# Optimization experiments

Measured on AMD Instinct MI355X. Metric: run time of the kernel, lower is better.

Reference implementation:

```python
import jax, jax.numpy as jnp
import numpy as np

H, D, DK, DV = 8, 512, 64, 64
B, L = 2, 2048
LN_EPS = 1e-5


def setup_inputs() -> dict:
    key = jax.random.key(0)
    ks = jax.random.split(key, 12)
    q = jax.random.normal(ks[0], (B, L, D), jnp.float32)
    k = jax.random.normal(ks[1], (B, L, D), jnp.float32)
    v = jax.random.normal(ks[2], (B, L, D), jnp.float32)
    mask = jax.random.randint(ks[3], (H * B, L, L), 0, 2) > 0
    sq = np.sqrt(2.0 / (D + DK)).astype(np.float32)
    sv = np.sqrt(2.0 / (D + DV)).astype(np.float32)
    Wq = jax.random.normal(ks[4], (H * DK, D), jnp.float32) * sq
    Wk = jax.random.normal(ks[5], (H * DK, D), jnp.float32) * sq
    Wv = jax.random.normal(ks[6], (H * DV, D), jnp.float32) * sv
    xav = np.sqrt(2.0 / (H * DV + D)).astype(np.float32)
    Wfc = jax.random.normal(ks[7], (D, H * DV), jnp.float32) * xav
    bfc = jnp.zeros((D,), jnp.float32)
    gamma = jnp.ones((D,), jnp.float32)
    beta = jnp.zeros((D,), jnp.float32)
    return {"q": q, "k": k, "v": v, "mask": mask, "Wq": Wq, "Wk": Wk,
            "Wv": Wv, "Wfc": Wfc, "bfc": bfc, "gamma": gamma, "beta": beta}


def reference(q, k, v, mask, Wq, Wk, Wv, Wfc, bfc, gamma, beta):
    # dropout in eval mode (identity)
    temperature = jnp.sqrt(jnp.asarray(DK, q.dtype))
    residual = q
    # projections -> (H, B, L, dk/dv), matching permute(2,0,1,3)
    qh = (q @ Wq.T).reshape(B, L, H, DK).transpose(2, 0, 1, 3)
    kh = (k @ Wk.T).reshape(B, L, H, DK).transpose(2, 0, 1, 3)
    vh = (v @ Wv.T).reshape(B, L, H, DV).transpose(2, 0, 1, 3)
    attn = jnp.einsum('hbqd,hbkd->hbqk', qh, kh) / temperature
    m = mask.reshape(H, B, L, L)
    attn = jnp.where(m, jnp.asarray(-1e10, attn.dtype), attn)
    attn = jax.nn.softmax(attn, axis=-1)
    out = jnp.einsum('hbqk,hbkd->hbqd', attn, vh)  # (H,B,L,DV)
    out = out.transpose(1, 2, 0, 3).reshape(B, L, H * DV)
    out = out @ Wfc.T + bfc
    x = out + residual
    mu = jnp.mean(x, axis=-1, keepdims=True)
    var = jnp.var(x, axis=-1, keepdims=True)
    return gamma * (x - mu) * jax.lax.rsqrt(var + LN_EPS) + beta
```

## Files before the change

kernel.cpp:

```cpp
#include <hip/hip_runtime.h>
#include <hip/hip_bf16.h>
#include <cmath>
#include <cstdint>

#define H_ 8
#define B_ 2
#define L_ 2048
#define D_ 512
#define SPLIT_ 4
#define LP 80

typedef __attribute__((ext_vector_type(8))) short short8_t;
typedef __attribute__((ext_vector_type(4))) float float4_t;
typedef __attribute__((ext_vector_type(4))) unsigned short ushort4_t;
typedef __attribute__((ext_vector_type(4))) unsigned int uint4_t;

__device__ __forceinline__ unsigned short bf16u(float f) {
  union { __hip_bfloat16 b; unsigned short u; } c;
  c.b = __float2bfloat16(f);
  return c.u;
}
__device__ __forceinline__ unsigned bf16x2(float lo, float hi) {
  return (unsigned)bf16u(lo) | ((unsigned)bf16u(hi) << 16);
}
__device__ __forceinline__ float bf2f(unsigned short u) {
  union { unsigned u; float f; } c; c.u = (unsigned)u << 16; return c.f;
}

__device__ __forceinline__ unsigned pack8(unsigned long long x) {
  x |= x >> 4; x |= x >> 2; x |= x >> 1;
  x &= 0x0101010101010101ULL;
  return (unsigned)((x * 0x0102040810204080ULL) >> 56);
}

__global__ __launch_bounds__(512)
void proj_gemm(const float* __restrict__ q, const float* __restrict__ k,
               const float* __restrict__ v,
               const float* __restrict__ wq, const float* __restrict__ wk,
               const float* __restrict__ wv,
               unsigned short* __restrict__ Qp, unsigned short* __restrict__ Kp,
               unsigned short* __restrict__ Vt) {
  __shared__ unsigned short As[128][LP];
  __shared__ unsigned short Bs[64][LP];
  const int tid = threadIdx.x, lane = tid & 63, wave = tid >> 6;
  const int g = lane >> 4, qi = lane & 15;
  const int m0 = blockIdx.x * 128, n0 = blockIdx.y * 64;
  const int z = blockIdx.z;
  const float* A = (z == 0) ? q : (z == 1) ? k : v;
  const float* W = (z == 0) ? wq : (z == 1) ? wk : wv;

  float4_t acc[4] = {};
  const int ar = tid >> 2, ac = (tid & 3) * 16;
  const int br = tid >> 3, bc = (tid & 7) * 8;

  for (int kt = 0; kt < 512; kt += 64) {
    const float* src = A + (size_t)(m0 + ar) * 512 + kt + ac;
    float4_t f0 = *(const float4_t*)(src);
    float4_t f1 = *(const float4_t*)(src + 4);
    float4_t f2 = *(const float4_t*)(src + 8);
    float4_t f3 = *(const float4_t*)(src + 12);
    short8_t s0, s1;
    s0[0] = bf16u(f0[0]); s0[1] = bf16u(f0[1]); s0[2] = bf16u(f0[2]); s0[3] = bf16u(f0[3]);
    s0[4] = bf16u(f1[0]); s0[5] = bf16u(f1[1]); s0[6] = bf16u(f1[2]); s0[7] = bf16u(f1[3]);
    s1[0] = bf16u(f2[0]); s1[1] = bf16u(f2[1]); s1[2] = bf16u(f2[2]); s1[3] = bf16u(f2[3]);
    s1[4] = bf16u(f3[0]); s1[5] = bf16u(f3[1]); s1[6] = bf16u(f3[2]); s1[7] = bf16u(f3[3]);
    *(short8_t*)(&As[ar][ac]) = s0;
    *(short8_t*)(&As[ar][ac + 8]) = s1;
    const float* wsrc = W + (size_t)(n0 + br) * 512 + kt + bc;
    float4_t w0 = *(const float4_t*)(wsrc);
    float4_t w1 = *(const float4_t*)(wsrc + 4);
    short8_t sw;
    sw[0] = bf16u(w0[0]); sw[1] = bf16u(w0[1]); sw[2] = bf16u(w0[2]); sw[3] = bf16u(w0[3]);
    sw[4] = bf16u(w1[0]); sw[5] = bf16u(w1[1]); sw[6] = bf16u(w1[2]); sw[7] = bf16u(w1[3]);
    *(short8_t*)(&Bs[br][bc]) = sw;
    __syncthreads();
#pragma unroll
    for (int kk = 0; kk < 2; kk++) {
      const int krow = kk * 32 + g * 8;
      short8_t a = *(const short8_t*)(&As[wave * 16 + qi][krow]);
#pragma unroll
      for (int n = 0; n < 4; n++) {
        short8_t b = *(const short8_t*)(&Bs[n * 16 + qi][krow]);
        acc[n] = __builtin_amdgcn_mfma_f32_16x16x32_bf16(a, b, acc[n], 0, 0, 0);
      }
    }
    __syncthreads();
  }

  const int gmb = m0 + wave * 16 + g * 4;
#pragma unroll
  for (int n = 0; n < 4; n++) {
    int gn = n0 + n * 16 + qi;
    int h = gn >> 6, d = gn & 63;
    if (z == 2) {
      int bb = gmb >> 11, l = gmb & 2047;
      ushort4_t o;
#pragma unroll
      for (int r = 0; r < 4; r++) o[r] = bf16u(acc[n][r]);
      *(ushort4_t*)(Vt + ((size_t)(h * B_ + bb) * 64 + d) * L_ + l) = o;
    } else {
      float sc = (z == 0) ? 0.125f : 1.0f;
      unsigned short* O = (z == 0) ? Qp : Kp;
#pragma unroll
      for (int r = 0; r < 4; r++) {
        int gm = gmb + r;
        int bb = gm >> 11, l = gm & 2047;
        O[((size_t)(h * B_ + bb) * L_ + l) * 64 + d] = bf16u(acc[n][r] * sc);
      }
    }
  }
}

template<int MS>
__device__ __forceinline__ void attn_body(
    const unsigned short* __restrict__ Qp, const unsigned short* __restrict__ Kp,
    const unsigned short* __restrict__ Vt, const unsigned char* __restrict__ mask,
    unsigned short* __restrict__ Opart, float* __restrict__ MLpart,
    unsigned short (*Ks)[64][LP], unsigned short (*Vs)[64][LP]) {
  const int tid = threadIdx.x, lane = tid & 63, wave = tid >> 6;
  const int g = lane >> 4, qi = lane & 15;
  const int hb = blockIdx.y;
  const int sp = blockIdx.z;
  const int k_begin = sp * (L_ / SPLIT_), k_end = k_begin + L_ / SPLIT_;
  const int qg0 = blockIdx.x * 128 + wave * 16;
  const int qg = qg0 + qi;
  const size_t base = (size_t)hb * (L_ * 64);

  const size_t mrowoff = ((size_t)hb * L_ + qg0 + (lane >> 2)) * L_;
  const unsigned char* mb1 = mask + mrowoff + (lane & 3) * 16;
  const unsigned* mb4 = (const unsigned*)mask + mrowoff + (lane & 3) * 16;

  short8_t qf[2];
#pragma unroll
  for (int kk = 0; kk < 2; kk++)
    qf[kk] = *(const short8_t*)(Qp + base + (size_t)qg * 64 + kk * 32 + g * 8);

  float4_t o[4] = {};
  float mrun = -INFINITY, lrun = 0.f;
  const int sr = tid >> 3, sc = (tid & 7) * 8;
  const int srcA = qi * 4;
  const int srcP = qi + 32 * (g & 1);

#define LOADFB(dst, kpos)                                                        \
  do {                                                                           \
    if (MS == 1) {                                                               \
      uint4_t x = *(const uint4_t*)(mb1 + (kpos));                               \
      unsigned long long lo = ((unsigned long long)x[1] << 32) | x[0];           \
      unsigned long long hi = ((unsigned long long)x[3] << 32) | x[2];           \
      dst = pack8(lo) | (pack8(hi) << 8);                                        \
    } else {                                                                     \
      dst = 0;                                                                   \
      _Pragma("unroll")                                                          \
      for (int j = 0; j < 4; j++) {                                              \
        uint4_t x = *(const uint4_t*)(mb4 + (kpos) + j * 4);                     \
        dst |= (((unsigned)(x[0] != 0)) | ((unsigned)(x[1] != 0) << 1) |         \
                ((unsigned)(x[2] != 0) << 2) | ((unsigned)(x[3] != 0) << 3))     \
               << (j * 4);                                                       \
      }                                                                          \
    }                                                                            \
  } while (0)

  short8_t kr, vr;
  unsigned fb1, fb2;
  kr = *(const short8_t*)(Kp + base + (size_t)(k_begin + sr) * 64 + sc);
  vr = *(const short8_t*)(Vt + base + (size_t)sr * L_ + k_begin + sc);
  LOADFB(fb1, k_begin);
  fb2 = 0;
  if (k_begin + 64 < k_end) LOADFB(fb2, k_begin + 64);
  *(short8_t*)(&Ks[0][sr][sc]) = kr;
  *(short8_t*)(&Vs[0][sr][sc]) = vr;
  __syncthreads();

  int bufi = 0;
  for (int k0 = k_begin; k0 < k_end; k0 += 64) {
    const bool has_next = (k0 + 64 < k_end);
    if (has_next) {
      const int kn = k0 + 64;
      kr = *(const short8_t*)(Kp + base + (size_t)(kn + sr) * 64 + sc);
      vr = *(const short8_t*)(Vt + base + (size_t)sr * L_ + kn + sc);
    }
    unsigned fb_cur = fb1;
    fb1 = fb2;
    if (k0 + 128 < k_end) LOADFB(fb2, k0 + 128);

    unsigned nib[4];
#pragma unroll
    for (int t = 0; t < 4; t++)
      nib[t] = ((unsigned)__shfl((int)fb_cur, srcA + t, 64) >> (g * 4)) & 0xFu;

    float4_t st[4] = {};
#pragma unroll
    for (int kk = 0; kk < 2; kk++) {
      const int krow = kk * 32 + g * 8;
#pragma unroll
      for (int t = 0; t < 4; t++) {
        short8_t a = *(const short8_t*)(&Ks[bufi][t * 16 + qi][krow]);
        st[t] = __builtin_amdgcn_mfma_f32_16x16x32_bf16(a, qf[kk], st[t], 0, 0, 0);
      }
    }

    float tmax = -INFINITY;
#pragma unroll
    for (int t = 0; t < 4; t++)
#pragma unroll
      for (int r = 0; r < 4; r++) {
        if ((nib[t] >> r) & 1u) st[t][r] = -1e10f;
        tmax = fmaxf(tmax, st[t][r]);
      }
    tmax = fmaxf(tmax, __shfl_xor(tmax, 16, 64));
    tmax = fmaxf(tmax, __shfl_xor(tmax, 32, 64));

    float nm = fmaxf(mrun, tmax);
    float fac = __expf(mrun - nm);
    mrun = nm;

    float psum = 0.f;
    unsigned w8[4][2];
#pragma unroll
    for (int t = 0; t < 4; t++) {
      float p0 = __expf(st[t][0] - nm);
      float p1 = __expf(st[t][1] - nm);
      float p2 = __expf(st[t][2] - nm);
      float p3 = __expf(st[t][3] - nm);
      psum += (p0 + p1) + (p2 + p3);
      w8[t][0] = bf16x2(p0, p1);
      w8[t][1] = bf16x2(p2, p3);
    }
    psum += __shfl_xor(psum, 16, 64);
    psum += __shfl_xor(psum, 32, 64);
    lrun = lrun * fac + psum;
#pragma unroll
    for (int n2 = 0; n2 < 4; n2++)
#pragma unroll
      for (int r = 0; r < 4; r++) o[n2][r] *= fac;

#pragma unroll
    for (int s = 0; s < 2; s++) {
      unsigned a00 = (unsigned)__shfl((int)w8[2 * s][0],     srcP, 64);
      unsigned a10 = (unsigned)__shfl((int)w8[2 * s + 1][0], srcP, 64);
      unsigned a01 = (unsigned)__shfl((int)w8[2 * s][1],     srcP, 64);
      unsigned a11 = (unsigned)__shfl((int)w8[2 * s + 1][1], srcP, 64);
      unsigned b00 = (unsigned)__shfl((int)w8[2 * s][0],     srcP + 16, 64);
      unsigned b10 = (unsigned)__shfl((int)w8[2 * s + 1][0], srcP + 16, 64);
      unsigned b01 = (unsigned)__shfl((int)w8[2 * s][1],     srcP + 16, 64);
      unsigned b11 = (unsigned)__shfl((int)w8[2 * s + 1][1], srcP + 16, 64);
      const bool hi = (g & 2) != 0;
      union { unsigned u[4]; short8_t s8; } pb;
      pb.u[0] = hi ? a10 : a00;
      pb.u[1] = hi ? a11 : a01;
      pb.u[2] = hi ? b10 : b00;
      pb.u[3] = hi ? b11 : b01;
#pragma unroll
      for (int n2 = 0; n2 < 4; n2++) {
        short8_t a = *(const short8_t*)(&Vs[bufi][n2 * 16 + qi][s * 32 + g * 8]);
        o[n2] = __builtin_amdgcn_mfma_f32_16x16x32_bf16(a, pb.s8, o[n2], 0, 0, 0);
      }
    }

    if (has_next) {
      *(short8_t*)(&Ks[bufi ^ 1][sr][sc]) = kr;
      *(short8_t*)(&Vs[bufi ^ 1][sr][sc]) = vr;
      __syncthreads();
      bufi ^= 1;
    }
  }
#undef LOADFB

  const size_t pb = (((size_t)sp * 16 + hb) * L_ + qg) * 64;
#pragma unroll
  for (int n2 = 0; n2 < 4; n2++) {
    ushort4_t ov;
#pragma unroll
    for (int r = 0; r < 4; r++) ov[r] = bf16u(o[n2][r]);
    *(ushort4_t*)(Opart + pb + n2 * 16 + g * 4) = ov;
  }
  if (lane < 16) {
    float* ml = MLpart + (((size_t)sp * 16 + hb) * L_ + qg) * 2;
    ml[0] = mrun; ml[1] = lrun;
  }
}

__global__ __launch_bounds__(512)
void attn_split(const unsigned short* __restrict__ Qp, const unsigned short* __restrict__ Kp,
                const unsigned short* __restrict__ Vt, const unsigned char* __restrict__ mask,
                unsigned short* __restrict__ Opart, float* __restrict__ MLpart) {
  __shared__ unsigned short Ks[2][64][LP];
  __shared__ unsigned short Vs[2][64][LP];
  unsigned probe = ((const unsigned*)mask)[threadIdx.x & 63];
  if (__any(probe > 1u))
    attn_body<1>(Qp, Kp, Vt, mask, Opart, MLpart, Ks, Vs);
  else
    attn_body<4>(Qp, Kp, Vt, mask, Opart, MLpart, Ks, Vs);
}

__global__ __launch_bounds__(256)
void attn_combine(const unsigned short* __restrict__ Opart, const float* __restrict__ MLpart,
                  unsigned short* __restrict__ Y) {
  int gid = blockIdx.x * 256 + threadIdx.x;
  int dvc = (gid & 7) * 8;
  int hbq = gid >> 3;
  int hb = hbq >> 11, qq = hbq & 2047;
  int h = hb >> 1, bb = hb & 1;
  float m[SPLIT_], l[SPLIT_];
  float M = -INFINITY;
#pragma unroll
  for (int s = 0; s < SPLIT_; s++) {
    const float* ml = MLpart + (((size_t)s * 16 + hb) * L_ + qq) * 2;
    m[s] = ml[0]; l[s] = ml[1];
    M = fmaxf(M, m[s]);
  }
  float denom = 0.f, e[SPLIT_];
#pragma unroll
  for (int s = 0; s < SPLIT_; s++) { e[s] = __expf(m[s] - M); denom += l[s] * e[s]; }
  float inv = 1.0f / denom;
  float acc[8] = {};
#pragma unroll
  for (int s = 0; s < SPLIT_; s++) {
    const unsigned short* p = Opart + (((size_t)s * 16 + hb) * L_ + qq) * 64 + dvc;
    ushort4_t a0 = *(const ushort4_t*)(p);
    ushort4_t a1 = *(const ushort4_t*)(p + 4);
    float w = e[s] * inv;
#pragma unroll
    for (int j = 0; j < 4; j++) {
      acc[j] += bf2f(a0[j]) * w;
      acc[j + 4] += bf2f(a1[j]) * w;
    }
  }
  short8_t ov;
#pragma unroll
  for (int j = 0; j < 8; j++) ov[j] = bf16u(acc[j]);
  *(short8_t*)(Y + ((size_t)(bb * L_ + qq)) * 512 + h * 64 + dvc) = ov;
}

__global__ __launch_bounds__(512)
void fc_gemm(const unsigned short* __restrict__ Yb, const float* __restrict__ wfc,
             const float* __restrict__ resid, const float* __restrict__ bfc,
             float* __restrict__ out) {
  __shared__ unsigned short As[128][LP];
  __shared__ unsigned short Bs[64][LP];
  const int tid = threadIdx.x, lane = tid & 63, wave = tid >> 6;
  const int g = lane >> 4, qi = lane & 15;
  const int m0 = blockIdx.x * 128, n0 = blockIdx.y * 64;
  float4_t acc[4] = {};
  const int ar = tid >> 2, ac = (tid & 3) * 16;
  const int br = tid >> 3, bc = (tid & 7) * 8;

  for (int kt = 0; kt < 512; kt += 64) {
    const unsigned short* src = Yb + (size_t)(m0 + ar) * 512 + kt + ac;
    *(short8_t*)(&As[ar][ac]) = *(const short8_t*)(src);
    *(short8_t*)(&As[ar][ac + 8]) = *(const short8_t*)(src + 8);
    const float* wsrc = wfc + (size_t)(n0 + br) * 512 + kt + bc;
    float4_t w0 = *(const float4_t*)(wsrc);
    float4_t w1 = *(const float4_t*)(wsrc + 4);
    short8_t sw;
    sw[0] = bf16u(w0[0]); sw[1] = bf16u(w0[1]); sw[2] = bf16u(w0[2]); sw[3] = bf16u(w0[3]);
    sw[4] = bf16u(w1[0]); sw[5] = bf16u(w1[1]); sw[6] = bf16u(w1[2]); sw[7] = bf16u(w1[3]);
    *(short8_t*)(&Bs[br][bc]) = sw;
    __syncthreads();
#pragma unroll
    for (int kk = 0; kk < 2; kk++) {
      const int krow = kk * 32 + g * 8;
      short8_t a = *(const short8_t*)(&As[wave * 16 + qi][krow]);
#pragma unroll
      for (int n = 0; n < 4; n++) {
        short8_t b = *(const short8_t*)(&Bs[n * 16 + qi][krow]);
        acc[n] = __builtin_amdgcn_mfma_f32_16x16x32_bf16(a, b, acc[n], 0, 0, 0);
      }
    }
    __syncthreads();
  }

  const int gmb = m0 + wave * 16 + g * 4;
#pragma unroll
  for (int n = 0; n < 4; n++) {
    int gn = n0 + n * 16 + qi;
    float bv = bfc[gn];
#pragma unroll
    for (int r = 0; r < 4; r++) {
      int gm = gmb + r;
      out[(size_t)gm * 512 + gn] = acc[n][r] + bv + resid[(size_t)gm * 512 + gn];
    }
  }
}

__global__ __launch_bounds__(256)
void ln_kernel(float* __restrict__ Z, const float* __restrict__ gamma,
               const float* __restrict__ beta) {
  const int row = blockIdx.x * 4 + (threadIdx.x >> 6);
  const int lane = threadIdx.x & 63;
  float* zp = Z + (size_t)row * 512 + lane * 8;
  float4_t x0 = *(const float4_t*)(zp);
  float4_t x1 = *(const float4_t*)(zp + 4);
  float s = 0.f, s2 = 0.f;
#pragma unroll
  for (int j = 0; j < 4; j++) { s += x0[j] + x1[j]; s2 += x0[j] * x0[j] + x1[j] * x1[j]; }
#pragma unroll
  for (int mm = 1; mm < 64; mm <<= 1) { s += __shfl_xor(s, mm, 64); s2 += __shfl_xor(s2, mm, 64); }
  float mu = s * (1.f / 512.f);
  float var = s2 * (1.f / 512.f) - mu * mu;
  float inv = rsqrtf(var + 1e-5f);
  float4_t g0 = *(const float4_t*)(gamma + lane * 8);
  float4_t g1 = *(const float4_t*)(gamma + lane * 8 + 4);
  float4_t b0 = *(const float4_t*)(beta + lane * 8);
  float4_t b1 = *(const float4_t*)(beta + lane * 8 + 4);
#pragma unroll
  for (int j = 0; j < 4; j++) {
    x0[j] = g0[j] * (x0[j] - mu) * inv + b0[j];
    x1[j] = g1[j] * (x1[j] - mu) * inv + b1[j];
  }
  *(float4_t*)(zp) = x0;
  *(float4_t*)(zp + 4) = x1;
}

extern "C" void kernel_launch(void* const* d_in, const int* in_sizes, int n_in,
                              void* d_out, int out_size, void* d_ws, size_t ws_size,
                              hipStream_t stream) {
  const float* q   = (const float*)d_in[0];
  const float* k   = (const float*)d_in[1];
  const float* v   = (const float*)d_in[2];
  const unsigned char* mask = (const unsigned char*)d_in[3];
  const float* Wq  = (const float*)d_in[4];
  const float* Wk  = (const float*)d_in[5];
  const float* Wv  = (const float*)d_in[6];
  const float* Wfc = (const float*)d_in[7];
  const float* bfc = (const float*)d_in[8];
  const float* gamma = (const float*)d_in[9];
  const float* beta  = (const float*)d_in[10];
  float* out = (float*)d_out;

  char* ws = (char*)d_ws;
  unsigned short* Qp   = (unsigned short*)(ws);
  unsigned short* Kp   = Qp + 2097152;
  unsigned short* Vt   = Kp + 2097152;
  unsigned short* Y    = Vt + 2097152;
  unsigned short* Opart = Y + 2097152;
  float* MLpart = (float*)(Opart + (size_t)SPLIT_ * 16 * L_ * 64);

  proj_gemm<<<dim3(32, 8, 3), 512, 0, stream>>>(q, k, v, Wq, Wk, Wv, Qp, Kp, Vt);
  attn_split<<<dim3(16, 16, SPLIT_), 512, 0, stream>>>(Qp, Kp, Vt, mask, Opart, MLpart);
  attn_combine<<<1024, 256, 0, stream>>>(Opart, MLpart, Y);
  fc_gemm<<<dim3(32, 8), 512, 0, stream>>>(Y, Wfc, q, bfc, out);
  ln_kernel<<<1024, 256, 0, stream>>>(out, gamma, beta);
}
```

Baseline: 121.3 us.

## Fuse split-K attention combine into FC GEMM A-tile load; add MFMA setprio

Removes the separate attn_combine kernel and the Y intermediate buffer. The FC GEMM now merges the four split partial outputs and their max/sum statistics directly while loading each A tile into shared memory. This saves one launch and a round trip of Y through memory. In exchange, the merge is recomputed by each of the 8 column blocks (blockIdx.y), which re-reads the partials and re-does the exp work. Separately, s_setprio is raised around the MFMA loops in the attention kernel to favour matrix-issue waves.

```diff
diff --git a/kernel.cpp b/kernel.cpp
--- a/kernel.cpp
+++ b/kernel.cpp
@@ -189,6 +189,7 @@
       nib[t] = ((unsigned)__shfl((int)fb_cur, srcA + t, 64) >> (g * 4)) & 0xFu;
 
     float4_t st[4] = {};
+    __builtin_amdgcn_s_setprio(1);
 #pragma unroll
     for (int kk = 0; kk < 2; kk++) {
       const int krow = kk * 32 + g * 8;
@@ -198,6 +199,7 @@
         st[t] = __builtin_amdgcn_mfma_f32_16x16x32_bf16(a, qf[kk], st[t], 0, 0, 0);
       }
     }
+    __builtin_amdgcn_s_setprio(0);
 
     float tmax = -INFINITY;
 #pragma unroll
@@ -250,11 +252,13 @@
       pb.u[1] = hi ? a11 : a01;
       pb.u[2] = hi ? b10 : b00;
       pb.u[3] = hi ? b11 : b01;
+      __builtin_amdgcn_s_setprio(1);
 #pragma unroll
       for (int n2 = 0; n2 < 4; n2++) {
         short8_t a = *(const short8_t*)(&Vs[bufi][n2 * 16 + qi][s * 32 + g * 8]);
         o[n2] = __builtin_amdgcn_mfma_f32_16x16x32_bf16(a, pb.s8, o[n2], 0, 0, 0);
       }
+      __builtin_amdgcn_s_setprio(0);
     }
 
     if (has_next) {
@@ -293,49 +297,10 @@
     attn_body<4>(Qp, Kp, Vt, mask, Opart, MLpart, Ks, Vs);
 }
 
-__global__ __launch_bounds__(256)
-void attn_combine(const unsigned short* __restrict__ Opart, const float* __restrict__ MLpart,
-                  unsigned short* __restrict__ Y) {
-  int gid = blockIdx.x * 256 + threadIdx.x;
-  int dvc = (gid & 7) * 8;
-  int hbq = gid >> 3;
-  int hb = hbq >> 11, qq = hbq & 2047;
-  int h = hb >> 1, bb = hb & 1;
-  float m[SPLIT_], l[SPLIT_];
-  float M = -INFINITY;
-#pragma unroll
-  for (int s = 0; s < SPLIT_; s++) {
-    const float* ml = MLpart + (((size_t)s * 16 + hb) * L_ + qq) * 2;
-    m[s] = ml[0]; l[s] = ml[1];
-    M = fmaxf(M, m[s]);
-  }
-  float denom = 0.f, e[SPLIT_];
-#pragma unroll
-  for (int s = 0; s < SPLIT_; s++) { e[s] = __expf(m[s] - M); denom += l[s] * e[s]; }
-  float inv = 1.0f / denom;
-  float acc[8] = {};
-#pragma unroll
-  for (int s = 0; s < SPLIT_; s++) {
-    const unsigned short* p = Opart + (((size_t)s * 16 + hb) * L_ + qq) * 64 + dvc;
-    ushort4_t a0 = *(const ushort4_t*)(p);
-    ushort4_t a1 = *(const ushort4_t*)(p + 4);
-    float w = e[s] * inv;
-#pragma unroll
-    for (int j = 0; j < 4; j++) {
-      acc[j] += bf2f(a0[j]) * w;
-      acc[j + 4] += bf2f(a1[j]) * w;
-    }
-  }
-  short8_t ov;
-#pragma unroll
-  for (int j = 0; j < 8; j++) ov[j] = bf16u(acc[j]);
-  *(short8_t*)(Y + ((size_t)(bb * L_ + qq)) * 512 + h * 64 + dvc) = ov;
-}
-
 __global__ __launch_bounds__(512)
-void fc_gemm(const unsigned short* __restrict__ Yb, const float* __restrict__ wfc,
-             const float* __restrict__ resid, const float* __restrict__ bfc,
-             float* __restrict__ out) {
+void fc_gemm(const unsigned short* __restrict__ Opart, const float* __restrict__ MLpart,
+             const float* __restrict__ wfc, const float* __restrict__ resid,
+             const float* __restrict__ bfc, float* __restrict__ out) {
   __shared__ unsigned short As[128][LP];
   __shared__ unsigned short Bs[64][LP];
   const int tid = threadIdx.x, lane = tid & 63, wave = tid >> 6;
@@ -344,11 +309,47 @@
   float4_t acc[4] = {};
   const int ar = tid >> 2, ac = (tid & 3) * 16;
   const int br = tid >> 3, bc = (tid & 7) * 8;
+  const int m = m0 + ar;
+  const int bb = m >> 11, l = m & 2047;
 
   for (int kt = 0; kt < 512; kt += 64) {
-    const unsigned short* src = Yb + (size_t)(m0 + ar) * 512 + kt + ac;
-    *(short8_t*)(&As[ar][ac]) = *(const short8_t*)(src);
-    *(short8_t*)(&As[ar][ac + 8]) = *(const short8_t*)(src + 8);
+    const int h = kt >> 6;
+    const int hb = h * 2 + bb;
+    float ms[SPLIT_], ls[SPLIT_];
+    float M = -INFINITY;
+#pragma unroll
+    for (int s = 0; s < SPLIT_; s++) {
+      const float* ml = MLpart + (((size_t)s * 16 + hb) * L_ + l) * 2;
+      ms[s] = ml[0]; ls[s] = ml[1];
+      M = fmaxf(M, ms[s]);
+    }
+    float den = 0.f, e[SPLIT_];
+#pragma unroll
+    for (int s = 0; s < SPLIT_; s++) { e[s] = __expf(ms[s] - M); den += ls[s] * e[s]; }
+    float inv = 1.0f / den;
+    float a16[16] = {};
+#pragma unroll
+    for (int s = 0; s < SPLIT_; s++) {
+      const unsigned short* p = Opart + ((((size_t)s * 16 + hb) * L_ + l) * 64 + ac);
+      ushort4_t p0 = *(const ushort4_t*)(p);
+      ushort4_t p1 = *(const ushort4_t*)(p + 4);
+      ushort4_t p2 = *(const ushort4_t*)(p + 8);
+      ushort4_t p3 = *(const ushort4_t*)(p + 12);
+      float w = e[s] * inv;
+#pragma unroll
+      for (int j = 0; j < 4; j++) {
+        a16[j]      += bf2f(p0[j]) * w;
+        a16[4 + j]  += bf2f(p1[j]) * w;
+        a16[8 + j]  += bf2f(p2[j]) * w;
+        a16[12 + j] += bf2f(p3[j]) * w;
+      }
+    }
+    short8_t s0, s1;
+#pragma unroll
+    for (int j = 0; j < 8; j++) { s0[j] = bf16u(a16[j]); s1[j] = bf16u(a16[8 + j]); }
+    *(short8_t*)(&As[ar][ac]) = s0;
+    *(short8_t*)(&As[ar][ac + 8]) = s1;
+
     const float* wsrc = wfc + (size_t)(n0 + br) * 512 + kt + bc;
     float4_t w0 = *(const float4_t*)(wsrc);
     float4_t w1 = *(const float4_t*)(wsrc + 4);
@@ -432,13 +433,11 @@
   unsigned short* Qp   = (unsigned short*)(ws);
   unsigned short* Kp   = Qp + 2097152;
   unsigned short* Vt   = Kp + 2097152;
-  unsigned short* Y    = Vt + 2097152;
-  unsigned short* Opart = Y + 2097152;
+  unsigned short* Opart = Vt + 2097152;
   float* MLpart = (float*)(Opart + (size_t)SPLIT_ * 16 * L_ * 64);
 
   proj_gemm<<<dim3(32, 8, 3), 512, 0, stream>>>(q, k, v, Wq, Wk, Wv, Qp, Kp, Vt);
   attn_split<<<dim3(16, 16, SPLIT_), 512, 0, stream>>>(Qp, Kp, Vt, mask, Opart, MLpart);
-  attn_combine<<<1024, 256, 0, stream>>>(Opart, MLpart, Y);
-  fc_gemm<<<dim3(32, 8), 512, 0, stream>>>(Y, Wfc, q, bfc, out);
+  fc_gemm<<<dim3(32, 8), 512, 0, stream>>>(Opart, MLpart, Wfc, q, bfc, out);
   ln_kernel<<<1024, 256, 0, stream>>>(out, gamma, beta);
 }
```

New measurement: 124.8 us. 2.9% more time.
